# Performance work log

Measured on AMD Instinct MI355X. Metric: run time of the kernel, lower is better.

The kernel has to match this reference:

```python
import jax, jax.numpy as jnp
import numpy as np
from jax import lax

N_NODES = 50000
N_EDGES = 800000
FEAT = 16
HID = 64
K = 32
N_CLASSES = 8


def _dconv(Xc, W, b, src, dst, norm_out, norm_in):
    """Dual-direction diffusion (Chebyshev-style) graph convolution.
    Xc: [N, Fin], W: [2, K, Fin, HID], norm_*: per-edge weights."""
    N = Xc.shape[0]

    def prop(x, s, d, ne):
        # out[i] = sum_{e: d[e]=i} ne[e] * x[s[e]]
        return jax.ops.segment_sum(x[s] * ne[:, None], d, num_segments=N)

    # k = 0 term (identity support, both directions)
    H = Xc @ (W[0, 0] + W[1, 0])
    # k = 1 term
    T1o = prop(Xc, src, dst, norm_out)   # forward diffusion
    T1i = prop(Xc, dst, src, norm_in)    # reverse diffusion
    H = H + T1o @ W[0, 1] + T1i @ W[1, 1]

    def step(carry, Wk):
        T0o, T1o, T0i, T1i, Hacc = carry
        T2o = 2.0 * prop(T1o, src, dst, norm_out) - T0o
        T2i = 2.0 * prop(T1i, dst, src, norm_in) - T0i
        Hacc = Hacc + T2o @ Wk[0] + T2i @ Wk[1]
        return (T1o, T2o, T1i, T2i, Hacc), None

    Wtail = jnp.stack([W[0, 2:], W[1, 2:]], axis=1)  # [K-2, 2, Fin, HID]
    (_, _, _, _, H), _ = lax.scan(step, (Xc, T1o, Xc, T1i, H), Wtail)
    return H + b


def setup_inputs() -> dict:
    key = jax.random.key(0)
    ks = jax.random.split(key, 8)
    Fin = FEAT + HID
    wscale = 1.0 / np.sqrt(Fin * K)
    x = jax.random.normal(ks[0], (N_NODES, FEAT), jnp.float32)
    edge_index = jax.random.randint(ks[1], (2, N_EDGES), 0, N_NODES, jnp.int64)
    W_z = jax.random.normal(ks[2], (2, K, Fin, HID), jnp.float32) * wscale
    W_r = jax.random.normal(ks[3], (2, K, Fin, HID), jnp.float32) * wscale
    W_h = jax.random.normal(ks[4], (2, K, Fin, HID), jnp.float32) * wscale
    lin_w = jax.random.normal(ks[5], (HID, N_CLASSES), jnp.float32) / np.sqrt(HID)
    return {
        "x": x, "edge_index": edge_index,
        "W_z": W_z, "b_z": jnp.zeros((HID,), jnp.float32),
        "W_r": W_r, "b_r": jnp.zeros((HID,), jnp.float32),
        "W_h": W_h, "b_h": jnp.zeros((HID,), jnp.float32),
        "lin_w": lin_w, "lin_b": jnp.zeros((N_CLASSES,), jnp.float32),
    }


def reference(x, edge_index, W_z, b_z, W_r, b_r, W_h, b_h, lin_w, lin_b):
    N = x.shape[0]
    src, dst = edge_index[0], edge_index[1]
    w = jnp.ones(src.shape[0], x.dtype)
    deg_out = jax.ops.segment_sum(w, src, num_segments=N)
    deg_in = jax.ops.segment_sum(w, dst, num_segments=N)
    inv = lambda d: jnp.where(d > 0, 1.0 / d, 0.0)
    norm_out = inv(deg_out)[src]  # per-edge 1/out-deg(source), forward walk
    norm_in = inv(deg_in)[dst]    # per-edge 1/in-deg(target), reverse walk

    # DCRNN GRU cell, single step, H initialized to zeros
    H0 = jnp.zeros((N, HID), x.dtype)
    Xc = jnp.concatenate([x, H0], axis=1)
    Z = jax.nn.sigmoid(_dconv(Xc, W_z, b_z, src, dst, norm_out, norm_in))
    R = jax.nn.sigmoid(_dconv(Xc, W_r, b_r, src, dst, norm_out, norm_in))
    Xh = jnp.concatenate([x, H0 * R], axis=1)
    Ht = jnp.tanh(_dconv(Xh, W_h, b_h, src, dst, norm_out, norm_in))
    H = Z * H0 + (1.0 - Z) * Ht

    return jax.nn.relu(H) @ lin_w + lin_b
```

## Files before the change

kernel.cpp:

```cpp
#include <hip/hip_runtime.h>
#include <math.h>

#define N_NODES 50000
#define N_EDGES 800000
#define FEAT    16
#define HID     64
#define KORD    32
#define NCLS    8

#define WSL     5120
#define SLOT    (N_NODES * FEAT)

typedef __attribute__((ext_vector_type(8))) short bf8_t;
typedef __attribute__((ext_vector_type(4))) float f32x4;

static constexpr size_t Aln(size_t x) { return (x + 255) & ~size_t(255); }

static constexpr size_t OFF_DEG_OUT = 0;
static constexpr size_t OFF_DEG_IN  = OFF_DEG_OUT + Aln(N_NODES * 4);
static constexpr size_t OFF_CUR_DST = OFF_DEG_IN  + Aln(N_NODES * 4);
static constexpr size_t OFF_CUR_SRC = OFF_CUR_DST + Aln(N_NODES * 4);
static constexpr size_t ZERO_BYTES  = OFF_CUR_SRC + Aln(N_NODES * 4);
static constexpr size_t OFF_OFF_DST = ZERO_BYTES;
static constexpr size_t OFF_OFF_SRC = OFF_OFF_DST + Aln((N_NODES + 1) * 4);
static constexpr size_t OFF_CSRD    = OFF_OFF_SRC + Aln((N_NODES + 1) * 4);
static constexpr size_t OFF_CSRS    = OFF_CSRD + Aln(N_EDGES * 4);
static constexpr size_t OFF_SLAB    = OFF_CSRS + Aln(N_EDGES * 4);
static constexpr size_t OFF_BSZH    = OFF_SLAB + Aln((size_t)64 * SLOT * 4);
static constexpr size_t OFF_BSZL    = OFF_BSZH + Aln((size_t)32 * 8 * 64 * 8 * 2);
static constexpr size_t WS_TOTAL    = OFF_BSZL + Aln((size_t)32 * 8 * 64 * 8 * 2);

__device__ __forceinline__ ushort f2bf(float v) {
    unsigned int b = __float_as_uint(v);
    b += 0x7FFFu + ((b >> 16) & 1u);
    return (ushort)(b >> 16);
}
__device__ __forceinline__ float bf2f(ushort h) {
    return __uint_as_float((unsigned int)h << 16);
}

__global__ void count_deg_kernel(const int* __restrict__ ei,
                                 int* __restrict__ deg_out, int* __restrict__ deg_in) {
    int e4 = blockIdx.x * blockDim.x + threadIdx.x;
    if (e4 * 4 >= N_EDGES) return;
    int4 s = *(const int4*)&ei[e4 * 4];
    int4 d = *(const int4*)&ei[N_EDGES + e4 * 4];
    atomicAdd(&deg_out[s.x], 1); atomicAdd(&deg_out[s.y], 1);
    atomicAdd(&deg_out[s.z], 1); atomicAdd(&deg_out[s.w], 1);
    atomicAdd(&deg_in[d.x], 1);  atomicAdd(&deg_in[d.y], 1);
    atomicAdd(&deg_in[d.z], 1);  atomicAdd(&deg_in[d.w], 1);
}

__global__ __launch_bounds__(1024) void scan_kernel(const int* __restrict__ degA, int* __restrict__ offA,
                                                    const int* __restrict__ degB, int* __restrict__ offB) {
    const int* deg = blockIdx.x ? degB : degA;
    int* off = blockIdx.x ? offB : offA;
    __shared__ int wsum[16];
    __shared__ int s_run;
    const int t = threadIdx.x, lane = t & 63, wid = t >> 6;
    if (t == 0) s_run = 0;
    __syncthreads();
    for (int base = 0; base < N_NODES; base += 1024) {
        int i = base + t;
        int v = (i < N_NODES) ? deg[i] : 0;
        int xv = v;
        #pragma unroll
        for (int d = 1; d < 64; d <<= 1) {
            int tt = __shfl_up(xv, d, 64);
            if (lane >= d) xv += tt;
        }
        if (lane == 63) wsum[wid] = xv;
        __syncthreads();
        int add = s_run;
        for (int w = 0; w < wid; ++w) add += wsum[w];
        if (i < N_NODES) off[i] = add + xv - v;
        __syncthreads();
        if (t == 1023) s_run = add + xv;
        __syncthreads();
    }
    if (t == 0) off[N_NODES] = s_run;
}

__global__ void fill_csr_kernel(const int* __restrict__ ei,
                                const int* __restrict__ deg_out, const int* __restrict__ deg_in,
                                const int* __restrict__ off_dst, const int* __restrict__ off_src,
                                int* __restrict__ cur_dst, int* __restrict__ cur_src,
                                unsigned int* __restrict__ csrd, unsigned int* __restrict__ csrs) {
    int e = blockIdx.x * blockDim.x + threadIdx.x;
    if (e >= N_EDGES) return;
    int s = ei[e], d = ei[N_EDGES + e];
    int p = off_dst[d] + atomicAdd(&cur_dst[d], 1);
    csrd[p] = ((unsigned int)deg_out[s] << 16) | (unsigned int)s;
    int q = off_src[s] + atomicAdd(&cur_src[s], 1);
    csrs[q] = ((unsigned int)deg_in[d] << 16) | (unsigned int)d;
}

__device__ __forceinline__ float4 gather4d(const unsigned int* __restrict__ csr, int beg, int end,
                                           int u, int fq, const float* __restrict__ src) {
    float4 acc = {0.f, 0.f, 0.f, 0.f};
    for (int e0 = beg; e0 < end; e0 += 16) {
        int ea = e0 + u, eb = e0 + 4 + u, ec = e0 + 8 + u, ed = e0 + 12 + u;
        unsigned int pa = (ea < end) ? csr[ea] : 0x10000u;
        unsigned int pb = (eb < end) ? csr[eb] : 0x10000u;
        unsigned int pc = (ec < end) ? csr[ec] : 0x10000u;
        unsigned int pd = (ed < end) ? csr[ed] : 0x10000u;
        float wa = (ea < end) ? 1.0f / (float)(pa >> 16) : 0.0f;
        float wb = (eb < end) ? 1.0f / (float)(pb >> 16) : 0.0f;
        float wc = (ec < end) ? 1.0f / (float)(pc >> 16) : 0.0f;
        float wd = (ed < end) ? 1.0f / (float)(pd >> 16) : 0.0f;
        const float4 ra = *(const float4*)&src[(pa & 0xFFFFu) * FEAT + fq * 4];
        const float4 rb = *(const float4*)&src[(pb & 0xFFFFu) * FEAT + fq * 4];
        const float4 rc = *(const float4*)&src[(pc & 0xFFFFu) * FEAT + fq * 4];
        const float4 rd = *(const float4*)&src[(pd & 0xFFFFu) * FEAT + fq * 4];
        acc.x += wa * ra.x + wb * rb.x + wc * rc.x + wd * rd.x;
        acc.y += wa * ra.y + wb * rb.y + wc * rc.y + wd * rd.y;
        acc.z += wa * ra.z + wb * rb.z + wc * rc.z + wd * rd.z;
        acc.w += wa * ra.w + wb * rb.w + wc * rc.w + wd * rd.w;
    }
    return acc;
}

__device__ __forceinline__ float4 reduce_u(float4 a) {
    a.x += __shfl_xor(a.x, 4); a.y += __shfl_xor(a.y, 4);
    a.z += __shfl_xor(a.z, 4); a.w += __shfl_xor(a.w, 4);
    a.x += __shfl_xor(a.x, 8); a.y += __shfl_xor(a.y, 8);
    a.z += __shfl_xor(a.z, 8); a.w += __shfl_xor(a.w, 8);
    return a;
}

__global__ __launch_bounds__(256) void init_kernel(
    const float* __restrict__ x,
    const int* __restrict__ off_dst, const unsigned int* __restrict__ csrd,
    const int* __restrict__ off_src, const unsigned int* __restrict__ csrs,
    float* __restrict__ slab) {
    const int dir = blockIdx.y;
    const int* off = dir ? off_src : off_dst;
    const unsigned int* csr = dir ? csrs : csrd;
    const int t = threadIdx.x;
    const int g = t >> 4, l = t & 15, u = l >> 2, fq = l & 3;
    const int i = blockIdx.x * 16 + g;
    const int b = off[i], e = off[i + 1];
    float4 a = reduce_u(gather4d(csr, b, e, u, fq, x));
    if (u == 0) {
        const int ro = i * FEAT + fq * 4;
        float4 xr = *(const float4*)&x[ro];
        *(float4*)&slab[(size_t)(dir * 32 + 0) * SLOT + ro] = xr;
        *(float4*)&slab[(size_t)(dir * 32 + 1) * SLOT + ro] = a;
    }
}

__global__ __launch_bounds__(256) void step_kernel(
    const int* __restrict__ off_dst, const unsigned int* __restrict__ csrd,
    const int* __restrict__ off_src, const unsigned int* __restrict__ csrs,
    float* __restrict__ slab, int k) {
    const int dir = blockIdx.y;
    const int* off = dir ? off_src : off_dst;
    const unsigned int* csr = dir ? csrs : csrd;
    const float* prev = slab + (size_t)(dir * 32 + k - 1) * SLOT;
    const float* pp   = slab + (size_t)(dir * 32 + k - 2) * SLOT;
    float*       outp = slab + (size_t)(dir * 32 + k) * SLOT;
    const int t = threadIdx.x;
    const int g = t >> 4, l = t & 15, u = l >> 2, fq = l & 3;
    const int i = blockIdx.x * 16 + g;
    const int b = off[i], e = off[i + 1];
    float4 a = reduce_u(gather4d(csr, b, e, u, fq, prev));
    if (u == 0) {
        const int ro = i * FEAT + fq * 4;
        float4 p = *(const float4*)&pp[ro];
        float4 t2;
        t2.x = 2.f * a.x - p.x; t2.y = 2.f * a.y - p.y;
        t2.z = 2.f * a.z - p.z; t2.w = 2.f * a.w - p.w;
        *(float4*)&outp[ro] = t2;
    }
}

__global__ void wswiz_kernel(const float* __restrict__ Wz, const float* __restrict__ Wh,
                             ushort* __restrict__ bszh, ushort* __restrict__ bszl) {
    int idx = blockIdx.x * blockDim.x + threadIdx.x;
    if (idx >= 32 * 8 * 64) return;
    int l  = idx & 63;
    int nc = (idx >> 6) & 7;
    int kc = idx >> 9;
    int si = kc * 2 + ((l >> 4) >> 1);
    int f0 = ((l >> 4) & 1) * 8;
    int c  = nc * 16 + (l & 15);
    const float* W = (c < 64) ? Wz : Wh;
    int cc = (c < 64) ? c : c - 64;
    ushort vh[8], vl[8];
    #pragma unroll
    for (int i = 0; i < 8; ++i) {
        float v = W[(size_t)si * WSL + (f0 + i) * 64 + cc];
        ushort h = f2bf(v);
        vh[i] = h;
        vl[i] = f2bf(v - bf2f(h));
    }
    ushort* dh = &bszh[(size_t)idx * 8];
    *(ushort4*)dh       = make_ushort4(vh[0], vh[1], vh[2], vh[3]);
    *(ushort4*)(dh + 4) = make_ushort4(vh[4], vh[5], vh[6], vh[7]);
    ushort* dl = &bszl[(size_t)idx * 8];
    *(ushort4*)dl       = make_ushort4(vl[0], vl[1], vl[2], vl[3]);
    *(ushort4*)(dl + 4) = make_ushort4(vl[4], vl[5], vl[6], vl[7]);
}

__global__ __launch_bounds__(256) void final_kernel(
    const float* __restrict__ slab, const ushort* __restrict__ bszh, const ushort* __restrict__ bszl,
    const float* __restrict__ bz, const float* __restrict__ bh,
    const float* __restrict__ lin_w, const float* __restrict__ lin_b,
    float* __restrict__ out) {
    const int t = threadIdx.x;
    const int w = t >> 6, l = t & 63;
    const int cl = l & 15, hi = l >> 4;
    const int n0 = blockIdx.x * 64 + w * 16;

    f32x4 acc[8];
    #pragma unroll
    for (int nc = 0; nc < 8; ++nc) {
        int c = nc * 16 + cl;
        float bias = (c < 64) ? bz[c] : bh[c - 64];
        acc[nc] = (f32x4){bias, bias, bias, bias};
    }

    const int nodeA = n0 + cl;
    const int aOk = (nodeA < N_NODES);
    const int siAdd = (hi >> 1);
    const int f0 = (hi & 1) * 8;

    for (int kc = 0; kc < 32; ++kc) {
        bf8_t aHi = (bf8_t)0, aLo = (bf8_t)0;
        if (aOk) {
            int si = kc * 2 + siAdd;
            const float* ap = &slab[(size_t)si * SLOT + nodeA * FEAT + f0];
            float4 a0 = *(const float4*)ap;
            float4 a1 = *(const float4*)(ap + 4);
            float av[8] = {a0.x, a0.y, a0.z, a0.w, a1.x, a1.y, a1.z, a1.w};
            #pragma unroll
            for (int i = 0; i < 8; ++i) {
                ushort h = f2bf(av[i]);
                aHi[i] = (short)h;
                aLo[i] = (short)f2bf(av[i] - bf2f(h));
            }
        }
        #pragma unroll
        for (int nc = 0; nc < 8; ++nc) {
            const size_t fo = (size_t)(((kc * 8 + nc) * 64) + l) * 8;
            bf8_t bHi = *(const bf8_t*)&bszh[fo];
            bf8_t bLo = *(const bf8_t*)&bszl[fo];
            acc[nc] = __builtin_amdgcn_mfma_f32_16x16x32_bf16(aHi, bHi, acc[nc], 0, 0, 0);
            acc[nc] = __builtin_amdgcn_mfma_f32_16x16x32_bf16(aLo, bHi, acc[nc], 0, 0, 0);
            acc[nc] = __builtin_amdgcn_mfma_f32_16x16x32_bf16(aHi, bLo, acc[nc], 0, 0, 0);
        }
    }

    float po[4][8];
    #pragma unroll
    for (int i = 0; i < 4; ++i)
        #pragma unroll
        for (int cls = 0; cls < 8; ++cls) po[i][cls] = 0.f;
    #pragma unroll
    for (int i = 0; i < 4; ++i) {
        #pragma unroll
        for (int nc = 0; nc < 4; ++nc) {
            float hz = acc[nc][i], hh = acc[nc + 4][i];
            float z  = 1.f / (1.f + __expf(-hz));
            float ht = tanhf(hh);
            float v  = fmaxf(0.f, (1.f - z) * ht);
            const float* lwr = &lin_w[(nc * 16 + cl) * 8];
            #pragma unroll
            for (int cls = 0; cls < 8; ++cls) po[i][cls] += v * lwr[cls];
        }
    }
    #pragma unroll
    for (int m = 1; m < 16; m <<= 1) {
        #pragma unroll
        for (int i = 0; i < 4; ++i)
            #pragma unroll
            for (int cls = 0; cls < 8; ++cls)
                po[i][cls] += __shfl_xor(po[i][cls], m, 16);
    }
    if (cl < 8) {
        #pragma unroll
        for (int i = 0; i < 4; ++i) {
            int node = n0 + hi * 4 + i;
            if (node < N_NODES) out[node * NCLS + cl] = po[i][cl] + lin_b[cl];
        }
    }
}

extern "C" void kernel_launch(void* const* d_in, const int* in_sizes, int n_in,
                              void* d_out, int out_size, void* d_ws, size_t ws_size,
                              hipStream_t stream) {
    const float* x   = (const float*)d_in[0];
    const int*   ei  = (const int*)d_in[1];
    const float* Wz  = (const float*)d_in[2];
    const float* bz  = (const float*)d_in[3];
    const float* Wh  = (const float*)d_in[6];
    const float* bh  = (const float*)d_in[7];
    const float* lw  = (const float*)d_in[8];
    const float* lb  = (const float*)d_in[9];
    float* out = (float*)d_out;
    char* ws = (char*)d_ws;

    int*  deg_out = (int*)(ws + OFF_DEG_OUT);
    int*  deg_in  = (int*)(ws + OFF_DEG_IN);
    int*  cur_dst = (int*)(ws + OFF_CUR_DST);
    int*  cur_src = (int*)(ws + OFF_CUR_SRC);
    int*  off_dst = (int*)(ws + OFF_OFF_DST);
    int*  off_src = (int*)(ws + OFF_OFF_SRC);
    unsigned int* csrd = (unsigned int*)(ws + OFF_CSRD);
    unsigned int* csrs = (unsigned int*)(ws + OFF_CSRS);
    float*  slab = (float*)(ws + OFF_SLAB);
    ushort* bszh = (ushort*)(ws + OFF_BSZH);
    ushort* bszl = (ushort*)(ws + OFF_BSZL);

    hipMemsetAsync(ws, 0, ZERO_BYTES, stream);

    const int EB = (N_EDGES + 255) / 256;
    const int NB16 = N_NODES / 16;
    count_deg_kernel<<<(N_EDGES / 4 + 255) / 256, 256, 0, stream>>>(ei, deg_out, deg_in);
    scan_kernel<<<2, 1024, 0, stream>>>(deg_in, off_dst, deg_out, off_src);
    fill_csr_kernel<<<EB, 256, 0, stream>>>(ei, deg_out, deg_in, off_dst, off_src,
                                            cur_dst, cur_src, csrd, csrs);
    wswiz_kernel<<<(32 * 8 * 64 + 255) / 256, 256, 0, stream>>>(Wz, Wh, bszh, bszl);
    init_kernel<<<dim3(NB16, 2), 256, 0, stream>>>(x, off_dst, csrd, off_src, csrs, slab);

    for (int k = 2; k < KORD; ++k)
        step_kernel<<<dim3(NB16, 2), 256, 0, stream>>>(off_dst, csrd, off_src, csrs, slab, k);

    final_kernel<<<(N_NODES + 63) / 64, 256, 0, stream>>>(slab, bszh, bszl, bz, bh, lw, lb, out);
}
```

Baseline: 849.5 us.

## Split final GEMM K-loop across two wave groups and add prefetch touch in step kernel

The final kernel now runs 512 threads per block. Two groups of four waves each handle half of the 32 Chebyshev-order chunks, and their partial accumulators are combined through shared memory before the activation and output projection. This doubles the parallelism per node tile, at the cost of an LDS reduction and a block barrier. Separately, each step_kernel block now loads a contiguous 2048-float chunk of the previous slab and discards it, apparently to warm the cache before the irregular gather. That load adds bandwidth and may be wasted traffic.

```diff
diff --git a/kernel.cpp b/kernel.cpp
--- a/kernel.cpp
+++ b/kernel.cpp
@@ -160,6 +160,16 @@
     const float* pp   = slab + (size_t)(dir * 32 + k - 2) * SLOT;
     float*       outp = slab + (size_t)(dir * 32 + k) * SLOT;
     const int t = threadIdx.x;
+
+    {
+        int chunk = blockIdx.x >> 3;
+        size_t base = (size_t)chunk * 2048;
+        const float4* wsrc = (const float4*)&prev[base];
+        float4 v0 = wsrc[t];
+        float4 v1 = wsrc[t + 256];
+        asm volatile("" :: "v"(v0.x), "v"(v1.x));
+    }
+
     const int g = t >> 4, l = t & 15, u = l >> 2, fq = l & 3;
     const int i = blockIdx.x * 16 + g;
     const int b = off[i], e = off[i + 1];
@@ -202,21 +212,26 @@
     *(ushort4*)(dl + 4) = make_ushort4(vl[4], vl[5], vl[6], vl[7]);
 }
 
-__global__ __launch_bounds__(256) void final_kernel(
+__global__ __launch_bounds__(512) void final_kernel(
     const float* __restrict__ slab, const ushort* __restrict__ bszh, const ushort* __restrict__ bszl,
     const float* __restrict__ bz, const float* __restrict__ bh,
     const float* __restrict__ lin_w, const float* __restrict__ lin_b,
     float* __restrict__ out) {
+    __shared__ float red[4][64][33];
     const int t = threadIdx.x;
     const int w = t >> 6, l = t & 63;
+    const int wh = w & 3, kh = w >> 2;
     const int cl = l & 15, hi = l >> 4;
-    const int n0 = blockIdx.x * 64 + w * 16;
+    const int n0 = blockIdx.x * 64 + wh * 16;
 
     f32x4 acc[8];
     #pragma unroll
     for (int nc = 0; nc < 8; ++nc) {
-        int c = nc * 16 + cl;
-        float bias = (c < 64) ? bz[c] : bh[c - 64];
+        float bias = 0.f;
+        if (kh == 0) {
+            int c = nc * 16 + cl;
+            bias = (c < 64) ? bz[c] : bh[c - 64];
+        }
         acc[nc] = (f32x4){bias, bias, bias, bias};
     }
 
@@ -225,7 +240,7 @@
     const int siAdd = (hi >> 1);
     const int f0 = (hi & 1) * 8;
 
-    for (int kc = 0; kc < 32; ++kc) {
+    for (int kc = kh * 16; kc < kh * 16 + 16; ++kc) {
         bf8_t aHi = (bf8_t)0, aLo = (bf8_t)0;
         if (aOk) {
             int si = kc * 2 + siAdd;
@@ -251,6 +266,21 @@
         }
     }
 
+    if (kh == 1) {
+        #pragma unroll
+        for (int nc = 0; nc < 8; ++nc)
+            #pragma unroll
+            for (int i = 0; i < 4; ++i)
+                red[wh][l][nc * 4 + i] = acc[nc][i];
+    }
+    __syncthreads();
+    if (kh == 1) return;
+    #pragma unroll
+    for (int nc = 0; nc < 8; ++nc)
+        #pragma unroll
+        for (int i = 0; i < 4; ++i)
+            acc[nc][i] += red[wh][l][nc * 4 + i];
+
     float po[4][8];
     #pragma unroll
     for (int i = 0; i < 4; ++i)
@@ -326,5 +356,5 @@
     for (int k = 2; k < KORD; ++k)
         step_kernel<<<dim3(NB16, 2), 256, 0, stream>>>(off_dst, csrd, off_src, csrs, slab, k);
 
-    final_kernel<<<(N_NODES + 63) / 64, 256, 0, stream>>>(slab, bszh, bszl, bz, bh, lw, lb, out);
-}
+    final_kernel<<<(N_NODES + 63) / 64, 512, 0, stream>>>(slab, bszh, bszl, bz, bh, lw, lb, out);
+}
```

Result: slower. 939.5 us (+10.6%).
